# Kernel tuning notes

Hardware: AMD Instinct MI355X
Metric: run time of the kernel (lower is better)

Reference implementation:

```python
import jax, jax.numpy as jnp
import numpy as np

DIM = 768
HEADS = 12
HEAD_DIM = DIM // HEADS  # 64
GRID = 48               # H = W = 48 tokens
RANK = 8                # LoRA rank


def setup_inputs() -> dict:
    key = jax.random.key(0)
    ks = jax.random.split(key, 20)
    s = 0.02
    inp = {
        "x": jax.random.normal(ks[0], (1, GRID, GRID, DIM), dtype=jnp.float32),
        "Wq": jax.random.normal(ks[1], (DIM, DIM), dtype=jnp.float32) * s,
        "bq": jax.random.normal(ks[2], (DIM,), dtype=jnp.float32) * s,
        "Wk": jax.random.normal(ks[3], (DIM, DIM), dtype=jnp.float32) * s,
        "bk": jax.random.normal(ks[4], (DIM,), dtype=jnp.float32) * s,
        "Wv": jax.random.normal(ks[5], (DIM, DIM), dtype=jnp.float32) * s,
        "bv": jax.random.normal(ks[6], (DIM,), dtype=jnp.float32) * s,
        "Wp": jax.random.normal(ks[7], (DIM, DIM), dtype=jnp.float32) * s,
        "bp": jax.random.normal(ks[8], (DIM,), dtype=jnp.float32) * s,
        "rel_pos_h": jax.random.normal(ks[9], (2 * GRID - 1, HEAD_DIM), dtype=jnp.float32) * s,
        "rel_pos_w": jax.random.normal(ks[10], (2 * GRID - 1, HEAD_DIM), dtype=jnp.float32) * s,
        "Aq": jax.random.normal(ks[11], (DIM, RANK), dtype=jnp.float32) * s,
        "Bq": jax.random.normal(ks[12], (RANK, DIM), dtype=jnp.float32) * s,
        "Ak": jax.random.normal(ks[13], (DIM, RANK), dtype=jnp.float32) * s,
        "Bk": jax.random.normal(ks[14], (RANK, DIM), dtype=jnp.float32) * s,
        "Av": jax.random.normal(ks[15], (DIM, RANK), dtype=jnp.float32) * s,
        "Bv": jax.random.normal(ks[16], (RANK, DIM), dtype=jnp.float32) * s,
    }
    return inp


def _get_rel_pos(size, rel_pos):
    # q_size == k_size == size, rel_pos has exactly 2*size-1 rows -> direct lookup
    idx = jnp.arange(size)[:, None] - jnp.arange(size)[None, :] + (size - 1)
    return rel_pos[idx]  # (size, size, head_dim)


def reference(x, Wq, bq, Wk, bk, Wv, bv, Wp, bp, rel_pos_h, rel_pos_w,
              Aq, Bq, Ak, Bk, Av, Bv):
    B, H, W, _ = x.shape
    N = H * W
    scale = HEAD_DIM ** -0.5

    # QKV projections + LoRA additions
    q = x @ Wq + bq + (x @ Aq) @ Bq
    k = x @ Wk + bk + (x @ Ak) @ Bk
    v = x @ Wv + bv + (x @ Av) @ Bv

    # (B, heads, N, head_dim)
    q = q.reshape(B, N, HEADS, HEAD_DIM).transpose(0, 2, 1, 3)
    k = k.reshape(B, N, HEADS, HEAD_DIM).transpose(0, 2, 1, 3)
    v = v.reshape(B, N, HEADS, HEAD_DIM).transpose(0, 2, 1, 3)

    attn = jnp.einsum('bhnc,bhmc->bhnm', q, k) * scale  # (B, heads, N, N)

    # Decomposed relative position bias (SAM add_decomposed_rel_pos)
    Rh = _get_rel_pos(H, rel_pos_h)  # (H, H, c)
    Rw = _get_rel_pos(W, rel_pos_w)  # (W, W, c)
    r_q = q.reshape(B, HEADS, H, W, HEAD_DIM)
    rel_h = jnp.einsum('bnhwc,hkc->bnhwk', r_q, Rh)  # (B, heads, H, W, H)
    rel_w = jnp.einsum('bnhwc,wkc->bnhwk', r_q, Rw)  # (B, heads, H, W, W)
    attn = (attn.reshape(B, HEADS, H, W, H, W)
            + rel_h[..., :, None] + rel_w[..., None, :]).reshape(B, HEADS, N, N)

    attn = jax.nn.softmax(attn, axis=-1)
    out = jnp.einsum('bhnm,bhmc->bhnc', attn, v)        # (B, heads, N, c)
    out = out.transpose(0, 2, 1, 3).reshape(B, H, W, DIM)
    return out @ Wp + bp
```

## Files before the change

### kernel.cpp

```cpp
#include <hip/hip_runtime.h>


#define DIM   768
#define HEADS 12
#define HD    64
#define NTOK  2304
#define RANK  8
#define GRD   48
#define CHUNKS 3
#define KEYS_PER_CHUNK 768
#define KT_PER 12
#define LOG2E 1.44269504088896f

typedef __attribute__((ext_vector_type(8))) short bf16x8;
typedef __attribute__((ext_vector_type(4))) float f32x4;
typedef unsigned short ushort_t;

__device__ __forceinline__ unsigned short f2bf(float x) {
    union { float f; unsigned u; } v; v.f = x;
    unsigned r = v.u + 0x7fffu + ((v.u >> 16) & 1u);
    return (unsigned short)(r >> 16);
}
__device__ __forceinline__ float bf2f(unsigned short h) {
    return __uint_as_float(((unsigned)h) << 16);
}
__device__ __forceinline__ void gload_lds16(const ushort_t* g, ushort_t* l) {
    __builtin_amdgcn_global_load_lds(
        (const __attribute__((address_space(1))) unsigned int*)g,
        (__attribute__((address_space(3))) unsigned int*)l, 16, 0, 0);
}

__global__ __launch_bounds__(256) void k_prep(
    const float* __restrict__ x, ushort_t* __restrict__ xb,
    const float* __restrict__ rph, const float* __restrict__ rpw,
    ushort_t* __restrict__ rphb, ushort_t* __restrict__ rpwb,
    const float* __restrict__ Wq, const float* __restrict__ Wk,
    const float* __restrict__ Wv, const float* __restrict__ Wp,
    const float* __restrict__ Aq, const float* __restrict__ Bq,
    const float* __restrict__ Ak, const float* __restrict__ Bk,
    const float* __restrict__ Av, const float* __restrict__ Bv,
    ushort_t* __restrict__ WT) {
    int bid = blockIdx.x, tid = threadIdx.x;

    if (bid < 1740) {
        if (bid < 1728) {
            int idx = (bid * 256 + tid) * 4;
            float4 v = *(const float4*)(x + idx);
            ushort4 o = make_ushort4(f2bf(v.x), f2bf(v.y), f2bf(v.z), f2bf(v.w));
            *(ushort4*)(xb + idx) = o;
        } else {
            int e = ((bid - 1728) * 256 + tid) * 4;
            const int TSZ = (2 * GRD - 1) * HD;
            if (e < TSZ) {
                float4 v = *(const float4*)(rph + e);
                ushort4 o = make_ushort4(f2bf(v.x), f2bf(v.y), f2bf(v.z), f2bf(v.w));
                *(ushort4*)(rphb + e) = o;
            } else if (e < 2 * TSZ) {
                float4 v = *(const float4*)(rpw + e - TSZ);
                ushort4 o = make_ushort4(f2bf(v.x), f2bf(v.y), f2bf(v.z), f2bf(v.w));
                *(ushort4*)(rpwb + e - TSZ) = o;
            }
        }
    }

    int kb = (bid % 24) * 32;
    int nb = (bid / 24) * 32;
    int sel = nb / DIM, nmod = nb % DIM;
    const float* W = (sel == 0) ? Wq : (sel == 1) ? Wk : (sel == 2) ? Wv : Wp;
    const float* A = (sel == 0) ? Aq : (sel == 1) ? Ak : Av;
    const float* B = (sel == 0) ? Bq : (sel == 1) ? Bk : Bv;
    __shared__ float T[32][33];
    for (int i = tid; i < 1024; i += 256) {
        int kl = i >> 5, nl = i & 31;
        float v = W[(kb + kl) * DIM + nmod + nl];
        if (sel < 3) {
            #pragma unroll
            for (int r = 0; r < RANK; r++)
                v += A[(kb + kl) * RANK + r] * B[r * DIM + nmod + nl];
        }
        T[kl][nl] = v;
    }
    __syncthreads();
    if (tid < 128) {
        int nl = tid >> 2, k8 = (tid & 3) * 8;
        ushort_t tmp[8];
        #pragma unroll
        for (int q = 0; q < 8; q++) tmp[q] = f2bf(T[k8 + q][nl]);
        *(uint4*)&WT[(size_t)(nb + nl) * DIM + kb + k8] = *(const uint4*)tmp;
    }
}

__global__ __launch_bounds__(256) void k_gemm_qkv(
    const ushort_t* __restrict__ xb, const ushort_t* __restrict__ WT,
    const float* __restrict__ bq, const float* __restrict__ bk,
    const float* __restrict__ bv,
    ushort_t* __restrict__ Qb, ushort_t* __restrict__ Kb,
    ushort_t* __restrict__ Vtb) {
    __shared__ __align__(16) ushort_t pool[12288];
    ushort_t* As0 = pool;
    ushort_t* As1 = pool + 4096;
    ushort_t* Bs0 = pool + 8192;
    ushort_t* Bs1 = pool + 10240;
    int tid = threadIdx.x;
    int wave = tid >> 6, lane = tid & 63, quad = lane >> 4, l16 = lane & 15;
    int wx = wave & 1, wy = wave >> 1;
    int nb = blockIdx.x * 64, mb = blockIdx.y * 128;

    f32x4 zero = {0.f, 0.f, 0.f, 0.f};
    f32x4 acc[4][2];
    #pragma unroll
    for (int i = 0; i < 4; i++)
        #pragma unroll
        for (int j = 0; j < 2; j++) acc[i][j] = zero;

    int rl = lane >> 2;
    int cl = (lane & 3) * 8;
    const ushort_t* gA = xb + (size_t)(mb + wave * 32 + rl) * DIM + cl;
    const ushort_t* gB = WT + (size_t)(nb + wave * 16 + rl) * DIM + cl;
    ushort_t* lA0 = As0 + (wave * 32) * 32;
    ushort_t* lA1 = As1 + (wave * 32) * 32;
    ushort_t* lB0 = Bs0 + (wave * 16) * 32;
    ushort_t* lB1 = Bs1 + (wave * 16) * 32;

    for (int k0 = 0; k0 < DIM; k0 += 64) {
        __syncthreads();
        gload_lds16(gA + k0,                 lA0);
        gload_lds16(gA + k0 + 16 * DIM,      lA0 + 16 * 32);
        gload_lds16(gA + k0 + 32,            lA1);
        gload_lds16(gA + k0 + 32 + 16 * DIM, lA1 + 16 * 32);
        gload_lds16(gB + k0,                 lB0);
        gload_lds16(gB + k0 + 32,            lB1);
        __syncthreads();
        #pragma unroll
        for (int p = 0; p < 2; p++) {
            const ushort_t* Ap = p ? As1 : As0;
            const ushort_t* Bp = p ? Bs1 : Bs0;
            bf16x8 af[4], bf[2];
            #pragma unroll
            for (int i = 0; i < 4; i++)
                af[i] = *(const bf16x8*)&Ap[(wy * 64 + i * 16 + l16) * 32 + quad * 8];
            #pragma unroll
            for (int j = 0; j < 2; j++)
                bf[j] = *(const bf16x8*)&Bp[(wx * 32 + j * 16 + l16) * 32 + quad * 8];
            #pragma unroll
            for (int i = 0; i < 4; i++)
                #pragma unroll
                for (int j = 0; j < 2; j++)
                    acc[i][j] = __builtin_amdgcn_mfma_f32_16x16x32_bf16(af[i], bf[j], acc[i][j], 0, 0, 0);
        }
    }

    int sel = nb / DIM;
    int rem0 = nb - sel * DIM;
    int hh = rem0 >> 6;
    const float* bias = (sel == 0) ? bq : (sel == 1) ? bk : bv;

    __syncthreads();

    if (sel < 2) {
        const int P = 72;
        #pragma unroll
        for (int j = 0; j < 2; j++) {
            int c = wx * 32 + j * 16 + l16;
            float bval = bias[rem0 + c];
            #pragma unroll
            for (int i = 0; i < 4; i++)
                #pragma unroll
                for (int r = 0; r < 4; r++) {
                    int row = wy * 64 + i * 16 + quad * 4 + r;
                    pool[row * P + c] = f2bf(acc[i][j][r] + bval);
                }
        }
        __syncthreads();
        ushort_t* qout = ((sel == 0) ? Qb : Kb) + (size_t)(hh * NTOK + mb) * HD;
        for (int idx = tid; idx < 128 * 8; idx += 256) {
            int row = idx >> 3, s8 = idx & 7;
            uint4 v = *(const uint4*)&pool[row * P + s8 * 8];
            *(uint4*)&qout[(size_t)row * HD + s8 * 8] = v;
        }
    } else {
        const int PV = 136;
        #pragma unroll
        for (int j = 0; j < 2; j++) {
            int c = wx * 32 + j * 16 + l16;
            float bval = bias[rem0 + c];
            #pragma unroll
            for (int i = 0; i < 4; i++)
                #pragma unroll
                for (int r = 0; r < 4; r++) {
                    int row = wy * 64 + i * 16 + quad * 4 + r;
                    pool[c * PV + row] = f2bf(acc[i][j][r] + bval);
                }
        }
        __syncthreads();
        ushort_t* vout = Vtb + (size_t)(hh * HD) * NTOK + mb;
        for (int idx = tid; idx < 64 * 16; idx += 256) {
            int cc = idx >> 4, r8 = idx & 15;
            uint4 v = *(const uint4*)&pool[cc * PV + r8 * 8];
            *(uint4*)&vout[(size_t)cc * NTOK + r8 * 8] = v;
        }
    }
}

__global__ __launch_bounds__(256) void k_relmm(
    const ushort_t* __restrict__ Qb, const ushort_t* __restrict__ rphb,
    const ushort_t* __restrict__ rpwb, float* __restrict__ relH,
    ushort_t* __restrict__ relWb) {
    int id = blockIdx.x * 4 + (threadIdx.x >> 6);
    int lane = threadIdx.x & 63, quad = lane >> 4, l16 = lane & 15;
    bool isW = id >= 1728;
    int t = isW ? id - 1728 : id;
    int ms = t % 3;
    int g  = (t / 3) % GRD;
    int h  = t / (3 * GRD);
    const ushort_t* tab = isW ? rpwb : rphb;

    f32x4 zero = {0.f, 0.f, 0.f, 0.f};
    f32x4 acc[3];
    #pragma unroll
    for (int ct = 0; ct < 3; ct++) acc[ct] = zero;

    bf16x8 bfr[3][2];
    #pragma unroll
    for (int ct = 0; ct < 3; ct++) {
        int trow = g + 47 - (ct * 16 + l16);
        bfr[ct][0] = *(const bf16x8*)&tab[(size_t)trow * HD + quad * 8];
        bfr[ct][1] = *(const bf16x8*)&tab[(size_t)trow * HD + 32 + quad * 8];
    }
    {
        int m = ms * 16 + l16;
        int n = isW ? m * GRD + g : g * GRD + m;
        bf16x8 a0 = *(const bf16x8*)&Qb[(size_t)(h * NTOK + n) * HD + quad * 8];
        bf16x8 a1 = *(const bf16x8*)&Qb[(size_t)(h * NTOK + n) * HD + 32 + quad * 8];
        #pragma unroll
        for (int ct = 0; ct < 3; ct++) {
            acc[ct] = __builtin_amdgcn_mfma_f32_16x16x32_bf16(a0, bfr[ct][0], acc[ct], 0, 0, 0);
            acc[ct] = __builtin_amdgcn_mfma_f32_16x16x32_bf16(a1, bfr[ct][1], acc[ct], 0, 0, 0);
        }
    }
    #pragma unroll
    for (int ct = 0; ct < 3; ct++) {
        #pragma unroll
        for (int r = 0; r < 4; r++) {
            int m = ms * 16 + quad * 4 + r;
            int n = isW ? m * GRD + g : g * GRD + m;
            int col = ct * 16 + l16;
            float val = acc[ct][r] * LOG2E;
            if (isW)
                relWb[(size_t)(h * NTOK + n) * GRD + col] = f2bf(val);
            else
                relH[(size_t)(h * NTOK + n) * GRD + col] = val;
        }
    }
}

__global__ __launch_bounds__(256, 3) void k_attn(
    const ushort_t* __restrict__ Qb, const ushort_t* __restrict__ Kb,
    const ushort_t* __restrict__ Vtb, const float* __restrict__ relH,
    const ushort_t* __restrict__ relWb, float* __restrict__ Opart,
    float* __restrict__ Lpart) {
    int h = blockIdx.x / CHUNKS, chunk = blockIdx.x - h * CHUNKS;
    int qt = blockIdx.y;
    int tid = threadIdx.x;
    int wave = tid >> 6, lane = tid & 63, quad = lane >> 4, l16 = lane & 15;
    int qbase = qt * 128;
    int kbase = chunk * KEYS_PER_CHUNK;

    __shared__ __align__(16) ushort_t Ks[64 * 68];
    __shared__ __align__(16) ushort_t Vs[64 * 68];
    __shared__ __align__(16) ushort_t Ps[4][32 * 68];
    __shared__ __align__(16) ushort_t rhs[128 * 18];

    for (int i = tid; i < 128 * 16; i += 256) {
        int r = i >> 4, c = i & 15;
        rhs[r * 18 + c] = f2bf(relH[(size_t)(h * NTOK + qbase + r) * GRD + chunk * 16 + c]);
    }

    bf16x8 qf[2][2];
    #pragma unroll
    for (int s = 0; s < 2; s++) {
        int qrow = qbase + wave * 32 + s * 16 + l16;
        qf[s][0] = *(const bf16x8*)&Qb[(size_t)(h * NTOK + qrow) * HD + quad * 8];
        qf[s][1] = *(const bf16x8*)&Qb[(size_t)(h * NTOK + qrow) * HD + 32 + quad * 8];
    }

    int r0 = tid >> 3, c0 = (tid & 7) * 8;
    const ushort_t* kg0 = Kb + (size_t)(h * NTOK + r0) * HD + c0;
    const ushort_t* kg1 = Kb + (size_t)(h * NTOK + r0 + 32) * HD + c0;
    const ushort_t* vg0 = Vtb + (size_t)(h * HD + r0) * NTOK + c0;
    const ushort_t* vg1 = Vtb + (size_t)(h * HD + r0 + 32) * NTOK + c0;
    int sk0 = r0 * 68 + c0, sk1 = sk0 + 32 * 68;

    const ushort_t* rw0 = relWb + (size_t)(h * NTOK + qbase + wave * 32 + l16) * GRD;
    const ushort_t* rw1 = rw0 + (size_t)16 * GRD;

    float lacc[2] = {0.f, 0.f};
    f32x4 zero = {0.f, 0.f, 0.f, 0.f};
    f32x4 oacc[2][4];
    #pragma unroll
    for (int s = 0; s < 2; s++)
        #pragma unroll
        for (int cs = 0; cs < 4; cs++) oacc[s][cs] = zero;

    const float scale2 = 0.125f * LOG2E;

    uint4 rk0 = *(const uint4*)(kg0 + (size_t)kbase * HD);
    uint4 rk1 = *(const uint4*)(kg1 + (size_t)kbase * HD);
    uint4 rv0 = *(const uint4*)(vg0 + kbase);
    uint4 rv1 = *(const uint4*)(vg1 + kbase);

    for (int kt = 0; kt < KT_PER; kt++) {
        int kb = kbase + kt * 64;

        __syncthreads();
        *(uint4*)&Ks[sk0] = rk0;  *(uint4*)&Ks[sk1] = rk1;
        *(uint4*)&Vs[sk0] = rv0;  *(uint4*)&Vs[sk1] = rv1;
        __syncthreads();

        uint2 rwv[2][4];
        #pragma unroll
        for (int ks = 0; ks < 4; ks++) {
            int kb4 = kb + ks * 16 + quad * 4;
            int kh = kb4 / 48;
            int kw0 = kb4 - kh * 48;
            rwv[0][ks] = *(const uint2*)(rw0 + kw0);
            rwv[1][ks] = *(const uint2*)(rw1 + kw0);
        }

        if (kt < KT_PER - 1) {
            int kbn = kb + 64;
            rk0 = *(const uint4*)(kg0 + (size_t)kbn * HD);
            rk1 = *(const uint4*)(kg1 + (size_t)kbn * HD);
            rv0 = *(const uint4*)(vg0 + kbn);
            rv1 = *(const uint4*)(vg1 + kbn);
        }

        #pragma unroll
        for (int ks = 0; ks < 4; ks++) {
            bf16x8 kf0 = *(const bf16x8*)&Ks[(ks * 16 + l16) * 68 + quad * 8];
            bf16x8 kf1 = *(const bf16x8*)&Ks[(ks * 16 + l16) * 68 + 32 + quad * 8];
            f32x4 st[2];
            __builtin_amdgcn_s_setprio(1);
            #pragma unroll
            for (int s = 0; s < 2; s++) {
                f32x4 z = zero;
                z = __builtin_amdgcn_mfma_f32_16x16x32_bf16(kf0, qf[s][0], z, 0, 0, 0);
                z = __builtin_amdgcn_mfma_f32_16x16x32_bf16(kf1, qf[s][1], z, 0, 0, 0);
                st[s] = z;
            }
            __builtin_amdgcn_s_setprio(0);
            int kb4 = kb + ks * 16 + quad * 4;
            int khl = kb4 / 48 - chunk * 16;
            #pragma unroll
            for (int s = 0; s < 2; s++) {
                int row = wave * 32 + s * 16 + l16;
                float rh = bf2f(rhs[row * 18 + khl]);
                uint2 u = rwv[s][ks];
                float p0 = __builtin_amdgcn_exp2f(st[s][0] * scale2 + rh + __uint_as_float(u.x << 16));
                float p1 = __builtin_amdgcn_exp2f(st[s][1] * scale2 + rh + __uint_as_float(u.x & 0xffff0000u));
                float p2 = __builtin_amdgcn_exp2f(st[s][2] * scale2 + rh + __uint_as_float(u.y << 16));
                float p3 = __builtin_amdgcn_exp2f(st[s][3] * scale2 + rh + __uint_as_float(u.y & 0xffff0000u));
                lacc[s] += (p0 + p1) + (p2 + p3);
                uint2 w;
                w.x = __builtin_amdgcn_perm(__float_as_uint(p1), __float_as_uint(p0), 0x07060302u);
                w.y = __builtin_amdgcn_perm(__float_as_uint(p3), __float_as_uint(p2), 0x07060302u);
                *(uint2*)&Ps[wave][(s * 16 + l16) * 68 + ks * 16 + quad * 4] = w;
            }
        }

        bf16x8 vf[4][2];
        #pragma unroll
        for (int cs = 0; cs < 4; cs++) {
            vf[cs][0] = *(const bf16x8*)&Vs[(cs * 16 + l16) * 68 + quad * 8];
            vf[cs][1] = *(const bf16x8*)&Vs[(cs * 16 + l16) * 68 + 32 + quad * 8];
        }
        __builtin_amdgcn_s_setprio(1);
        #pragma unroll
        for (int s = 0; s < 2; s++) {
            bf16x8 pa0 = *(const bf16x8*)&Ps[wave][(s * 16 + l16) * 68 + quad * 8];
            bf16x8 pa1 = *(const bf16x8*)&Ps[wave][(s * 16 + l16) * 68 + 32 + quad * 8];
            #pragma unroll
            for (int cs = 0; cs < 4; cs++) {
                oacc[s][cs] = __builtin_amdgcn_mfma_f32_16x16x32_bf16(pa0, vf[cs][0], oacc[s][cs], 0, 0, 0);
                oacc[s][cs] = __builtin_amdgcn_mfma_f32_16x16x32_bf16(pa1, vf[cs][1], oacc[s][cs], 0, 0, 0);
            }
        }
        __builtin_amdgcn_s_setprio(0);
    }

    #pragma unroll
    for (int s = 0; s < 2; s++) {
        float l = lacc[s];
        l += __shfl_xor(l, 16);
        l += __shfl_xor(l, 32);
        lacc[s] = l;
    }

    size_t obase = (size_t)(chunk * HEADS + h) * NTOK;
    #pragma unroll
    for (int s = 0; s < 2; s++) {
        #pragma unroll
        for (int cs = 0; cs < 4; cs++) {
            #pragma unroll
            for (int r = 0; r < 4; r++) {
                int row = qbase + wave * 32 + s * 16 + quad * 4 + r;
                Opart[(obase + row) * HD + cs * 16 + l16] = oacc[s][cs][r];
            }
        }
        if (quad == 0)
            Lpart[obase + qbase + wave * 32 + s * 16 + l16] = lacc[s];
    }
}

__global__ __launch_bounds__(256) void k_merge(const float* __restrict__ Opart,
                                               const float* __restrict__ Lpart,
                                               ushort_t* __restrict__ Ob) {
    int t = blockIdx.x * 256 + threadIdx.x;
    int e = t * 4;
    int c = e & (HD - 1);
    int row = (e >> 6) % NTOK;
    int h = e / (NTOK * HD);
    const int ostride = HEADS * NTOK * HD;
    float4 s = {0.f, 0.f, 0.f, 0.f};
    float l = 0.f;
    #pragma unroll
    for (int ch = 0; ch < CHUNKS; ch++) {
        float4 v = *(const float4*)&Opart[(size_t)ch * ostride + e];
        s.x += v.x; s.y += v.y; s.z += v.z; s.w += v.w;
        l += Lpart[(size_t)(ch * HEADS + h) * NTOK + row];
    }
    float inv = 1.0f / l;
    ushort4 o = make_ushort4(f2bf(s.x * inv), f2bf(s.y * inv),
                             f2bf(s.z * inv), f2bf(s.w * inv));
    *(ushort4*)&Ob[(size_t)row * DIM + h * HD + c] = o;
}

__global__ __launch_bounds__(256) void k_gemm_proj(
    const ushort_t* __restrict__ Ob, const ushort_t* __restrict__ WTp,
    const float* __restrict__ bp, float* __restrict__ out) {
    __shared__ __align__(16) ushort_t As[2][64 * 32];
    __shared__ __align__(16) ushort_t Bs[2][64 * 32];
    int tid = threadIdx.x;
    int wave = tid >> 6, lane = tid & 63, quad = lane >> 4, l16 = lane & 15;
    int wx = wave & 1, wy = wave >> 1;
    int nb = blockIdx.x * 64, mb = blockIdx.y * 64;

    f32x4 zero = {0.f, 0.f, 0.f, 0.f};
    f32x4 acc[2][2];
    #pragma unroll
    for (int i = 0; i < 2; i++)
        #pragma unroll
        for (int j = 0; j < 2; j++) acc[i][j] = zero;

    int rl = lane >> 2;
    int cl = (lane & 3) * 8;
    const ushort_t* gA = Ob + (size_t)(mb + wave * 16 + rl) * DIM + cl;
    const ushort_t* gB = WTp + (size_t)(nb + wave * 16 + rl) * DIM + cl;
    ushort_t* lA0 = &As[0][(wave * 16) * 32];
    ushort_t* lA1 = &As[1][(wave * 16) * 32];
    ushort_t* lB0 = &Bs[0][(wave * 16) * 32];
    ushort_t* lB1 = &Bs[1][(wave * 16) * 32];

    for (int k0 = 0; k0 < DIM; k0 += 64) {
        __syncthreads();
        gload_lds16(gA + k0,      lA0);
        gload_lds16(gA + k0 + 32, lA1);
        gload_lds16(gB + k0,      lB0);
        gload_lds16(gB + k0 + 32, lB1);
        __syncthreads();
        #pragma unroll
        for (int p = 0; p < 2; p++) {
            bf16x8 af[2], bf[2];
            #pragma unroll
            for (int i = 0; i < 2; i++)
                af[i] = *(const bf16x8*)&As[p][(wy * 32 + i * 16 + l16) * 32 + quad * 8];
            #pragma unroll
            for (int j = 0; j < 2; j++)
                bf[j] = *(const bf16x8*)&Bs[p][(wx * 32 + j * 16 + l16) * 32 + quad * 8];
            #pragma unroll
            for (int i = 0; i < 2; i++)
                #pragma unroll
                for (int j = 0; j < 2; j++)
                    acc[i][j] = __builtin_amdgcn_mfma_f32_16x16x32_bf16(af[i], bf[j], acc[i][j], 0, 0, 0);
        }
    }

    #pragma unroll
    for (int j = 0; j < 2; j++) {
        int col = nb + wx * 32 + j * 16 + l16;
        float bval = bp[col];
        #pragma unroll
        for (int i = 0; i < 2; i++) {
            #pragma unroll
            for (int r = 0; r < 4; r++) {
                int row = mb + wy * 32 + i * 16 + quad * 4 + r;
                out[(size_t)row * DIM + col] = acc[i][j][r] + bval;
            }
        }
    }
}

extern "C" void kernel_launch(void* const* d_in, const int* in_sizes, int n_in,
                              void* d_out, int out_size, void* d_ws, size_t ws_size,
                              hipStream_t stream) {
    const float* x   = (const float*)d_in[0];
    const float* Wq  = (const float*)d_in[1];
    const float* bq  = (const float*)d_in[2];
    const float* Wk  = (const float*)d_in[3];
    const float* bk  = (const float*)d_in[4];
    const float* Wv  = (const float*)d_in[5];
    const float* bv  = (const float*)d_in[6];
    const float* Wp  = (const float*)d_in[7];
    const float* bp  = (const float*)d_in[8];
    const float* rph = (const float*)d_in[9];
    const float* rpw = (const float*)d_in[10];
    const float* Aq  = (const float*)d_in[11];
    const float* Bq  = (const float*)d_in[12];
    const float* Ak  = (const float*)d_in[13];
    const float* Bk  = (const float*)d_in[14];
    const float* Av  = (const float*)d_in[15];
    const float* Bv  = (const float*)d_in[16];
    float* out = (float*)d_out;

    char* w = (char*)d_ws;
    size_t off = 0;
    auto carve = [&](size_t bytes) {
        char* p = w + off;
        off += (bytes + 255) & ~(size_t)255;
        return p;
    };
    ushort_t* xb    = (ushort_t*)carve((size_t)NTOK * DIM * 2);
    ushort_t* WT    = (ushort_t*)carve((size_t)4 * DIM * DIM * 2);
    ushort_t* Qb    = (ushort_t*)carve((size_t)HEADS * NTOK * HD * 2);
    ushort_t* Kb    = (ushort_t*)carve((size_t)HEADS * NTOK * HD * 2);
    ushort_t* Vtb   = (ushort_t*)carve((size_t)HEADS * HD * NTOK * 2);
    float*    relH  = (float*)carve((size_t)HEADS * NTOK * GRD * 4);
    ushort_t* relWb = (ushort_t*)carve((size_t)HEADS * NTOK * GRD * 2);
    ushort_t* Ob    = (ushort_t*)carve((size_t)NTOK * DIM * 2);
    float*    Opart = (float*)carve((size_t)CHUNKS * HEADS * NTOK * HD * 4);
    float*    Lpart = (float*)carve((size_t)CHUNKS * HEADS * NTOK * 4);
    ushort_t* rphb  = (ushort_t*)carve((size_t)(2 * GRD - 1) * HD * 2);
    ushort_t* rpwb  = (ushort_t*)carve((size_t)(2 * GRD - 1) * HD * 2);

    k_prep<<<dim3(2304), dim3(256), 0, stream>>>(
        x, xb, rph, rpw, rphb, rpwb,
        Wq, Wk, Wv, Wp, Aq, Bq, Ak, Bk, Av, Bv, WT);
    k_gemm_qkv<<<dim3(36, 18), dim3(256), 0, stream>>>(
        xb, WT, bq, bk, bv, Qb, Kb, Vtb);
    k_relmm<<<dim3(864), dim3(256), 0, stream>>>(
        Qb, rphb, rpwb, relH, relWb);
    k_attn<<<dim3(HEADS * CHUNKS, NTOK / 128), dim3(256), 0, stream>>>(
        Qb, Kb, Vtb, relH, relWb, Opart, Lpart);
    k_merge<<<dim3(HEADS * NTOK * HD / (256 * 4)), dim3(256), 0, stream>>>(
        Opart, Lpart, Ob);
    k_gemm_proj<<<dim3(12, 36), dim3(256), 0, stream>>>(
        Ob, WT + (size_t)3 * DIM * DIM, bp, out);
}
```

Baseline: 177.4 us.

## Double-buffer LDS staging in QKV and projection GEMMs; hoist key index division

Both GEMM kernels now keep two LDS stages. The next K-tile's global-to-LDS loads are issued before the current tile's MFMAs, and explicit vmcnt waits plus raw barriers replace the two __syncthreads per iteration, so memory latency overlaps compute. In attention, the per-tile division by 48 that gave key row and column indices is replaced by an incremental counter. The cost is doubled LDS footprint in the GEMMs, which may lower occupancy, and correctness now relies on hand-counted vmcnt values matching the number of outstanding loads.

```diff
diff --git a/kernel.cpp b/kernel.cpp
--- a/kernel.cpp
+++ b/kernel.cpp
@@ -96,11 +96,8 @@
     const float* __restrict__ bv,
     ushort_t* __restrict__ Qb, ushort_t* __restrict__ Kb,
     ushort_t* __restrict__ Vtb) {
-    __shared__ __align__(16) ushort_t pool[12288];
-    ushort_t* As0 = pool;
-    ushort_t* As1 = pool + 4096;
-    ushort_t* Bs0 = pool + 8192;
-    ushort_t* Bs1 = pool + 10240;
+    __shared__ __align__(16) ushort_t As[2][2][128 * 32];
+    __shared__ __align__(16) ushort_t Bs[2][2][64 * 32];
     int tid = threadIdx.x;
     int wave = tid >> 6, lane = tid & 63, quad = lane >> 4, l16 = lane & 15;
     int wx = wave & 1, wy = wave >> 1;
@@ -117,39 +114,45 @@
     int cl = (lane & 3) * 8;
     const ushort_t* gA = xb + (size_t)(mb + wave * 32 + rl) * DIM + cl;
     const ushort_t* gB = WT + (size_t)(nb + wave * 16 + rl) * DIM + cl;
-    ushort_t* lA0 = As0 + (wave * 32) * 32;
-    ushort_t* lA1 = As1 + (wave * 32) * 32;
-    ushort_t* lB0 = Bs0 + (wave * 16) * 32;
-    ushort_t* lB1 = Bs1 + (wave * 16) * 32;
-
-    for (int k0 = 0; k0 < DIM; k0 += 64) {
-        __syncthreads();
-        gload_lds16(gA + k0,                 lA0);
-        gload_lds16(gA + k0 + 16 * DIM,      lA0 + 16 * 32);
-        gload_lds16(gA + k0 + 32,            lA1);
-        gload_lds16(gA + k0 + 32 + 16 * DIM, lA1 + 16 * 32);
-        gload_lds16(gB + k0,                 lB0);
-        gload_lds16(gB + k0 + 32,            lB1);
-        __syncthreads();
+
+    auto stage = [&](int k0, int b) {
+        gload_lds16(gA + k0,                 &As[b][0][(wave * 32) * 32]);
+        gload_lds16(gA + k0 + 16 * DIM,      &As[b][0][(wave * 32) * 32] + 16 * 32);
+        gload_lds16(gA + k0 + 32,            &As[b][1][(wave * 32) * 32]);
+        gload_lds16(gA + k0 + 32 + 16 * DIM, &As[b][1][(wave * 32) * 32] + 16 * 32);
+        gload_lds16(gB + k0,                 &Bs[b][0][(wave * 16) * 32]);
+        gload_lds16(gB + k0 + 32,            &Bs[b][1][(wave * 16) * 32]);
+    };
+
+    stage(0, 0);
+    for (int it = 0; it < 12; ++it) {
+        int cur = it & 1;
+        if (it < 11) {
+            stage((it + 1) * 64, cur ^ 1);
+            asm volatile("s_waitcnt vmcnt(6)" ::: "memory");
+        } else {
+            asm volatile("s_waitcnt vmcnt(0)" ::: "memory");
+        }
+        __builtin_amdgcn_s_barrier();
         #pragma unroll
         for (int p = 0; p < 2; p++) {
-            const ushort_t* Ap = p ? As1 : As0;
-            const ushort_t* Bp = p ? Bs1 : Bs0;
             bf16x8 af[4], bf[2];
             #pragma unroll
             for (int i = 0; i < 4; i++)
-                af[i] = *(const bf16x8*)&Ap[(wy * 64 + i * 16 + l16) * 32 + quad * 8];
+                af[i] = *(const bf16x8*)&As[cur][p][(wy * 64 + i * 16 + l16) * 32 + quad * 8];
             #pragma unroll
             for (int j = 0; j < 2; j++)
-                bf[j] = *(const bf16x8*)&Bp[(wx * 32 + j * 16 + l16) * 32 + quad * 8];
+                bf[j] = *(const bf16x8*)&Bs[cur][p][(wx * 32 + j * 16 + l16) * 32 + quad * 8];
             #pragma unroll
             for (int i = 0; i < 4; i++)
                 #pragma unroll
                 for (int j = 0; j < 2; j++)
                     acc[i][j] = __builtin_amdgcn_mfma_f32_16x16x32_bf16(af[i], bf[j], acc[i][j], 0, 0, 0);
         }
-    }
-
+        __builtin_amdgcn_s_barrier();
+    }
+
+    ushort_t* pool = &As[0][0][0];
     int sel = nb / DIM;
     int rem0 = nb - sel * DIM;
     int hh = rem0 >> 6;
@@ -309,8 +312,23 @@
     uint4 rv0 = *(const uint4*)(vg0 + kbase);
     uint4 rv1 = *(const uint4*)(vg1 + kbase);
 
+    int kwS = quad * 4;
+    int khlS = 0;
+
     for (int kt = 0; kt < KT_PER; kt++) {
         int kb = kbase + kt * 64;
+
+        int kwA[4], khlA[4];
+        kwA[0] = kwS; khlA[0] = khlS;
+        #pragma unroll
+        for (int ks = 1; ks < 4; ks++) {
+            int kw = kwA[ks - 1] + 16, kh = khlA[ks - 1];
+            if (kw >= 48) { kw -= 48; kh += 1; }
+            kwA[ks] = kw; khlA[ks] = kh;
+        }
+        { int kw = kwA[3] + 16, kh = khlA[3];
+          if (kw >= 48) { kw -= 48; kh += 1; }
+          kwS = kw; khlS = kh; }
 
         __syncthreads();
         *(uint4*)&Ks[sk0] = rk0;  *(uint4*)&Ks[sk1] = rk1;
@@ -320,11 +338,8 @@
         uint2 rwv[2][4];
         #pragma unroll
         for (int ks = 0; ks < 4; ks++) {
-            int kb4 = kb + ks * 16 + quad * 4;
-            int kh = kb4 / 48;
-            int kw0 = kb4 - kh * 48;
-            rwv[0][ks] = *(const uint2*)(rw0 + kw0);
-            rwv[1][ks] = *(const uint2*)(rw1 + kw0);
+            rwv[0][ks] = *(const uint2*)(rw0 + kwA[ks]);
+            rwv[1][ks] = *(const uint2*)(rw1 + kwA[ks]);
         }
 
         if (kt < KT_PER - 1) {
@@ -349,8 +364,7 @@
                 st[s] = z;
             }
             __builtin_amdgcn_s_setprio(0);
-            int kb4 = kb + ks * 16 + quad * 4;
-            int khl = kb4 / 48 - chunk * 16;
+            int khl = khlA[ks];
             #pragma unroll
             for (int s = 0; s < 2; s++) {
                 int row = wave * 32 + s * 16 + l16;
@@ -438,8 +452,8 @@
 __global__ __launch_bounds__(256) void k_gemm_proj(
     const ushort_t* __restrict__ Ob, const ushort_t* __restrict__ WTp,
     const float* __restrict__ bp, float* __restrict__ out) {
-    __shared__ __align__(16) ushort_t As[2][64 * 32];
-    __shared__ __align__(16) ushort_t Bs[2][64 * 32];
+    __shared__ __align__(16) ushort_t As[2][2][64 * 32];
+    __shared__ __align__(16) ushort_t Bs[2][2][64 * 32];
     int tid = threadIdx.x;
     int wave = tid >> 6, lane = tid & 63, quad = lane >> 4, l16 = lane & 15;
     int wx = wave & 1, wy = wave >> 1;
@@ -456,33 +470,40 @@
     int cl = (lane & 3) * 8;
     const ushort_t* gA = Ob + (size_t)(mb + wave * 16 + rl) * DIM + cl;
     const ushort_t* gB = WTp + (size_t)(nb + wave * 16 + rl) * DIM + cl;
-    ushort_t* lA0 = &As[0][(wave * 16) * 32];
-    ushort_t* lA1 = &As[1][(wave * 16) * 32];
-    ushort_t* lB0 = &Bs[0][(wave * 16) * 32];
-    ushort_t* lB1 = &Bs[1][(wave * 16) * 32];
-
-    for (int k0 = 0; k0 < DIM; k0 += 64) {
-        __syncthreads();
-        gload_lds16(gA + k0,      lA0);
-        gload_lds16(gA + k0 + 32, lA1);
-        gload_lds16(gB + k0,      lB0);
-        gload_lds16(gB + k0 + 32, lB1);
-        __syncthreads();
+
+    auto stage = [&](int k0, int b) {
+        gload_lds16(gA + k0,      &As[b][0][(wave * 16) * 32]);
+        gload_lds16(gA + k0 + 32, &As[b][1][(wave * 16) * 32]);
+        gload_lds16(gB + k0,      &Bs[b][0][(wave * 16) * 32]);
+        gload_lds16(gB + k0 + 32, &Bs[b][1][(wave * 16) * 32]);
+    };
+
+    stage(0, 0);
+    for (int it = 0; it < 12; ++it) {
+        int cur = it & 1;
+        if (it < 11) {
+            stage((it + 1) * 64, cur ^ 1);
+            asm volatile("s_waitcnt vmcnt(4)" ::: "memory");
+        } else {
+            asm volatile("s_waitcnt vmcnt(0)" ::: "memory");
+        }
+        __builtin_amdgcn_s_barrier();
         #pragma unroll
         for (int p = 0; p < 2; p++) {
             bf16x8 af[2], bf[2];
             #pragma unroll
             for (int i = 0; i < 2; i++)
-                af[i] = *(const bf16x8*)&As[p][(wy * 32 + i * 16 + l16) * 32 + quad * 8];
+                af[i] = *(const bf16x8*)&As[cur][p][(wy * 32 + i * 16 + l16) * 32 + quad * 8];
             #pragma unroll
             for (int j = 0; j < 2; j++)
-                bf[j] = *(const bf16x8*)&Bs[p][(wx * 32 + j * 16 + l16) * 32 + quad * 8];
+                bf[j] = *(const bf16x8*)&Bs[cur][p][(wx * 32 + j * 16 + l16) * 32 + quad * 8];
             #pragma unroll
             for (int i = 0; i < 2; i++)
                 #pragma unroll
                 for (int j = 0; j < 2; j++)
                     acc[i][j] = __builtin_amdgcn_mfma_f32_16x16x32_bf16(af[i], bf[j], acc[i][j], 0, 0, 0);
         }
+        __builtin_amdgcn_s_barrier();
     }
 
     #pragma unroll
```

Result: no change. 173.9 us (median of 4 runs) (-2.0%).
